# Performance work log

Measured on AMD Instinct MI355X. Metric: run time of the kernel, lower is better.

## Reference

```python
import jax, jax.numpy as jnp
import numpy as np

K = 5              # B-spline kernel size per dim
K3 = K ** 3        # 125 kernel weight slots
B = 32             # graphs per batch
NPG = [2048, 512, 128, 32, 8]   # nodes per graph at each level
DEG = 16           # average degree
RS = [0.1, 0.1, 0.125, 0.25, 0.5]  # CartesianAdj radii (1/10,1/10,2/16,2/8,2/4)


def _edges(rng, npg):
    # random edges, constrained within each graph
    E = B * npg * DEG
    g = np.repeat(np.arange(B) * npg, npg * DEG)
    src = g + rng.integers(0, npg, E)
    dst = g + rng.integers(0, npg, E)
    return jnp.asarray(np.stack([src, dst]), jnp.int32)


def _cluster(npg_prev, npg):
    # balanced voxel-cluster assignment within each graph (every cluster non-empty)
    n = np.arange(B * npg_prev)
    return jnp.asarray((n // npg_prev) * npg + (n % npg_prev) % npg, jnp.int32)


def setup_inputs() -> dict:
    key = jax.random.key(0)
    ks = iter(jax.random.split(key, 64))
    rng = np.random.default_rng(0)
    d = {}
    d['x0'] = jax.random.normal(next(ks), (B * NPG[0], 1), jnp.float32)
    d['pos0'] = jax.random.uniform(next(ks), (B * NPG[0], 3), jnp.float32) * 2.0
    chans = [1, 32, 64, 96, 128, 256]
    for i in range(5):
        ci, co = chans[i], chans[i + 1]
        s = 1.0 / np.sqrt(ci)
        d[f'W{i+1}'] = jax.random.normal(next(ks), (K3, ci, co), jnp.float32) * s
        d[f'root{i+1}'] = jax.random.normal(next(ks), (ci, co), jnp.float32) * s
        d[f'b{i+1}'] = jax.random.normal(next(ks), (co,), jnp.float32) * 0.01
    for i, c in enumerate([32, 64, 96, 128]):
        d[f'Wa{i+1}'] = jax.random.normal(next(ks), (c, 2), jnp.float32) / np.sqrt(c)
        d[f'ba{i+1}'] = jnp.zeros((2,), jnp.float32)
    d['Wfc'] = jax.random.normal(next(ks), (8 * 256, 10), jnp.float32) * 0.02
    d['bfc'] = jnp.zeros((10,), jnp.float32)
    for i in range(5):
        d[f'ei{i}'] = _edges(rng, NPG[i])
    for i in range(4):
        d[f'c{i+1}'] = _cluster(NPG[i], NPG[i + 1])
    return d


def _cartesian(pos, ei, r):
    # CartesianAdj: relative edge offsets scaled to [0,1]
    delta = pos[ei[1]] - pos[ei[0]]
    return jnp.clip(delta / (2.0 * r) + 0.5, 0.0, 1.0)


def _spline_conv(x, ei, pseudo, W, root, b):
    # SplineConv, degree-1 open B-splines, dim=3, kernel_size=5, mean aggregation
    src, dst = ei[0], ei[1]
    N, Cin = x.shape
    u = pseudo * (K - 1)                       # [E,3]
    k0f = jnp.clip(jnp.floor(u), 0.0, K - 2)
    frac = u - k0f
    k0 = k0f.astype(jnp.int32)
    xs = x[src]                                # [E,Cin]
    A = jnp.zeros((N, K3, Cin), x.dtype)       # basis-weighted aggregation buffer
    for bits in range(8):                      # 2^3 corners of the spline support
        off = np.array([(bits >> t) & 1 for t in range(3)])
        w = jnp.prod(jnp.where(off[None, :] == 1, frac, 1.0 - frac), axis=1)  # [E]
        kd = k0 + off[None, :]
        kidx = kd[:, 0] + K * kd[:, 1] + K * K * kd[:, 2]
        A = A.at[dst, kidx].add(w[:, None] * xs)
    out = jnp.einsum('nki,kio->no', A, W)
    deg = jnp.zeros((N,), x.dtype).at[dst].add(1.0)
    return out / jnp.maximum(deg, 1.0)[:, None] + x @ root + b


def _max_pool(x, weight, pos, cluster, nc):
    # attention-weighted sparse voxel max pool: keep node with max weight per voxel
    n = x.shape[0]
    m = jax.ops.segment_max(weight, cluster, nc)
    cand = jnp.where(weight >= m[cluster], jnp.arange(n), n)
    sel = jnp.minimum(jax.ops.segment_min(cand, cluster, nc), n - 1)
    cnt = jax.ops.segment_sum(jnp.ones((n,), pos.dtype), cluster, nc)
    ppos = jax.ops.segment_sum(pos, cluster, nc) / jnp.maximum(cnt, 1.0)[:, None]
    return x[sel], ppos


def _forward(x0, pos0, Ws, roots, bs, Was, bas, Wfc, bfc, eis, cs):
    x, pos = x0, pos0
    for i in range(4):
        ps = _cartesian(pos, eis[i], RS[i])
        x = jax.nn.elu(_spline_conv(x, eis[i], ps, Ws[i], roots[i], bs[i]))
        att = x @ Was[i] + bas[i]
        x, pos = _max_pool(x, att[:, 0], pos, cs[i], B * NPG[i + 1])
    ps = _cartesian(pos, eis[4], RS[4])
    x = jax.nn.elu(_spline_conv(x, eis[4], ps, Ws[4], roots[4], bs[4]))
    # dense_voxel_max_pool(data, 1, -0.5, 1.5): 2x2x2 voxels per graph
    vox = jnp.clip(jnp.floor(pos + 0.5), 0, 1).astype(jnp.int32)
    batch = jnp.arange(B * NPG[4], dtype=jnp.int32) // NPG[4]
    cl = batch * 8 + vox[:, 0] * 4 + vox[:, 1] * 2 + vox[:, 2]
    mx = jax.ops.segment_max(x, cl, B * 8)
    cnt = jax.ops.segment_sum(jnp.ones((x.shape[0],), x.dtype), cl, B * 8)
    mx = jnp.where(cnt[:, None] > 0, mx, 0.0)  # empty voxels -> 0
    logits = mx.reshape(B, 8 * 256) @ Wfc + bfc  # eval mode: dropout is identity
    return jax.nn.log_softmax(logits, axis=1)


def reference(x0, pos0, W1, root1, b1, W2, root2, b2, W3, root3, b3, W4, root4, b4, W5, root5, b5, Wa1, ba1, Wa2, ba2, Wa3, ba3, Wa4, ba4, Wfc, bfc, ei0, ei1, ei2, ei3, ei4, c1, c2, c3, c4):
    return _forward(x0, pos0, [W1, W2, W3, W4, W5], [root1, root2, root3, root4, root5],
                    [b1, b2, b3, b4, b5], [Wa1, Wa2, Wa3, Wa4], [ba1, ba2, ba3, ba4],
                    Wfc, bfc, [ei0, ei1, ei2, ei3, ei4], [c1, c2, c3, c4])
```

## Files before the change

kernel.cpp:

```cpp
#include <hip/hip_runtime.h>
#include <hip/hip_bf16.h>
#include <cstdint>
#include <cstddef>

#define KS 5
#define K3 125

typedef __attribute__((ext_vector_type(8))) short bf16x8;
typedef __attribute__((ext_vector_type(4))) float f32x4;

struct PreArgs {
    const int* src[5]; const int* dst[5];
    int* cnt[5]; int* slots[5];
    int npg[5];
    const float* W[5]; unsigned short* Wt[5];
    int Kd[5], KdP[5], Co[5];
    int fillFirst[6]; int wtFirst[6]; int ktiles[5];
};

__device__ __forceinline__ unsigned f2ord(float f){
    unsigned u = __float_as_uint(f);
    return (u & 0x80000000u) ? ~u : (u | 0x80000000u);
}
__device__ __forceinline__ float ord2f(unsigned u){
    unsigned b = (u & 0x80000000u) ? (u & 0x7FFFFFFFu) : ~u;
    return __uint_as_float(b);
}
__device__ __forceinline__ unsigned short f2bf(float f){
    unsigned u = __float_as_uint(f);
    u = (u + 0x7FFFu + ((u >> 16) & 1u)) >> 16;
    return (unsigned short)u;
}
__device__ __forceinline__ unsigned pk_bf16(float a, float b){
    __hip_bfloat162 p = __float22bfloat162_rn(make_float2(a, b));
    return *(unsigned*)&p;
}

__global__ __launch_bounds__(1024) void k_pre3(PreArgs a){
    __shared__ float smf[64*65];
    int b = blockIdx.x;
    int tid = threadIdx.x;
    if(b < a.fillFirst[5]){
        int l = 0;
        while(b >= a.fillFirst[l+1]) l++;
        int g = b - a.fillFirst[l];
        int npg = a.npg[l];
        int E1 = npg*16;
        int nbase = g*npg;
        int* cnt = (int*)smf;
        for(int i=tid; i<npg; i+=1024) cnt[i] = 0;
        __syncthreads();
        const int* srcp = a.src[l] + (size_t)g*E1;
        const int* dstp = a.dst[l] + (size_t)g*E1;
        int* slots = a.slots[l];
        for(int e=tid; e<E1; e+=1024){
            int d = dstp[e];
            int s = srcp[e];
            int p = __hip_atomic_fetch_add(&cnt[d - nbase], 1,
                        __ATOMIC_RELAXED, __HIP_MEMORY_SCOPE_WORKGROUP);
            if(p < 64) slots[(size_t)d*64 + p] = s;
        }
        __syncthreads();
        int* cg = a.cnt[l];
        for(int i=tid; i<npg; i+=1024) cg[nbase + i] = cnt[i];
        return;
    }
    int r = b - a.fillFirst[5];
    int l = 0;
    while(r >= a.wtFirst[l+1]) l++;
    int idx = r - a.wtFirst[l];
    int kb = (idx % a.ktiles[l])*64;
    int cb = (idx / a.ktiles[l])*64;
    int Kd = a.Kd[l], KdP = a.KdP[l], Co = a.Co[l];
    const float* W = a.W[l];
    unsigned short* Wt = a.Wt[l];
    float (*t)[65] = (float(*)[65])smf;
    int cc = tid & 63, rg = tid >> 6;
    #pragma unroll
    for(int i=0;i<4;i++){
        int kl = rg + i*16;
        int kk = kb + kl, co = cb + cc;
        t[kl][cc] = (kk < Kd && co < Co) ? W[(size_t)kk*Co + co] : 0.f;
    }
    __syncthreads();
    int kl = tid & 63;
    #pragma unroll
    for(int i=0;i<4;i++){
        int col = rg + i*16;
        int co = cb + col;
        int kk = kb + kl;
        if(co < Co && kk < KdP) Wt[(size_t)co*KdP + kk] = f2bf(t[kl][col]);
    }
}

__device__ __forceinline__ void spline_meta(float dx, float dy, float dz, float inv2r,
        float* wgt, int* ki){
    float fr[3]; int k0[3];
    float dd[3] = {dx, dy, dz};
    #pragma unroll
    for(int dim=0; dim<3; dim++){
        float p = dd[dim]*inv2r + 0.5f;
        p = fminf(fmaxf(p, 0.f), 1.f);
        float u = p*4.0f;
        float kf = fminf(floorf(u), 3.f);
        fr[dim] = u - kf; k0[dim] = (int)kf;
    }
    #pragma unroll
    for(int bits=0; bits<8; bits++){
        wgt[bits] = ((bits&1)? fr[0] : 1.f-fr[0])
                  * ((bits&2)? fr[1] : 1.f-fr[1])
                  * ((bits&4)? fr[2] : 1.f-fr[2]);
        ki[bits]  = (k0[0]+(bits&1)) + KS*(k0[1]+((bits>>1)&1)) + KS*KS*(k0[2]+((bits>>2)&1));
    }
}

__global__ __launch_bounds__(256) void k_build2(const int* __restrict__ slots,
        const int* __restrict__ cnt, const float* __restrict__ pos,
        const float* __restrict__ x,
        float inv2r, int n0, int Cin, int KdP, unsigned short* __restrict__ A){
    const int CH = 32;
    __shared__ float row[K3*32];
    __shared__ float xbuf[CH*32];
    __shared__ float ew[CH][8];
    __shared__ unsigned short bkt[16][CH];
    __shared__ int bcnt[16];
    __shared__ int esrc[CH];
    int tid = threadIdx.x;
    int node = n0 + blockIdx.x;
    int ci0 = blockIdx.y*32;
    for(int i=tid; i<K3*32; i+=256) row[i] = 0.f;
    int ecnt = min(cnt[node], 64);
    const int* sl = slots + (size_t)node*64;
    float pdx = pos[node*3+0], pdy = pos[node*3+1], pdz = pos[node*3+2];

    for(int c0=0; c0<ecnt; c0+=CH){
        int cc2 = min(CH, ecnt-c0);
        __syncthreads();
        if(tid < 16) bcnt[tid] = 0;
        float w[8]; int ki[8];
        if(tid < cc2){
            int s = sl[c0+tid];
            esrc[tid] = s;
            spline_meta(pdx-pos[s*3+0], pdy-pos[s*3+1], pdz-pos[s*3+2], inv2r, w, ki);
            #pragma unroll
            for(int b=0;b<8;b++) ew[tid][b] = w[b];
        }
        __syncthreads();
        if(tid < cc2){
            #pragma unroll
            for(int b=0;b<8;b++){
                int g = ki[b] & 15;
                int p = atomicAdd(&bcnt[g], 1);
                bkt[g][p] = (unsigned short)((ki[b]<<8) | (tid<<3) | b);
            }
        }
        for(int i=tid; i<cc2*32; i+=256){
            int e = i >> 5, ci = i & 31;
            xbuf[i] = x[(size_t)esrc[e]*Cin + ci0 + ci];
        }
        __syncthreads();
        int g  = tid >> 4;
        int cl = (tid & 15)*2;
        int ng = bcnt[g];
        for(int i=0; i<ng; i++){
            unsigned v = bkt[g][i];
            int kq = v >> 8;
            int e  = (v >> 3) & 31;
            float wv = ew[e][v & 7];
            float2 xv = *(float2*)&xbuf[e*32 + cl];
            float2* rp = (float2*)&row[kq*32 + cl];
            float2 rv = *rp;
            rv.x += wv*xv.x;
            rv.y += wv*xv.y;
            *rp = rv;
        }
    }
    __syncthreads();
    size_t gbase = (size_t)blockIdx.x*KdP + ci0;
    for(int i=tid*4; i<K3*32; i+=1024){
        int k = i >> 5, c = i & 31;
        uint2 pk;
        pk.x = pk_bf16(row[i],   row[i+1]);
        pk.y = pk_bf16(row[i+2], row[i+3]);
        *(uint2*)&A[gbase + (size_t)k*Cin + c] = pk;
    }
}

__global__ __launch_bounds__(256) void k_build1(const int* __restrict__ slots,
        const int* __restrict__ cnt, const float* __restrict__ pos,
        const float* __restrict__ x,
        float inv2r, int n0, int KdP, unsigned short* __restrict__ A){
    const int NB = 32, KD = K3;
    __shared__ float rows[NB*KD];
    int tid = threadIdx.x;
    for(int i=tid; i<NB*KD; i+=256) rows[i] = 0.f;
    __syncthreads();
    int nb = tid >> 3;
    int grp = tid & 7;
    int node = n0 + blockIdx.x*NB + nb;
    float* row = rows + nb*KD;
    float pdx = pos[node*3+0], pdy = pos[node*3+1], pdz = pos[node*3+2];
    int ecnt = min(cnt[node], 64);
    const int* sl = slots + (size_t)node*64;
    for(int ii=grp; ii<ecnt; ii+=8){
        int s = sl[ii];
        float w[8]; int ki[8];
        spline_meta(pdx-pos[s*3+0], pdy-pos[s*3+1], pdz-pos[s*3+2], inv2r, w, ki);
        float xs = x[s];
        #pragma unroll
        for(int b=0; b<8; b++)
            __hip_atomic_fetch_add(&row[ki[b]], w[b]*xs, __ATOMIC_RELAXED, __HIP_MEMORY_SCOPE_WORKGROUP);
    }
    __syncthreads();
    size_t gbase = (size_t)blockIdx.x*NB*KdP;
    int tot = NB*KdP;
    for(int i=tid*2; i<tot; i+=512){
        int nbw = i / KdP;
        int kk  = i - nbw*KdP;
        float v0 = (kk   < KD) ? rows[nbw*KD + kk]   : 0.f;
        float v1 = (kk+1 < KD) ? rows[nbw*KD + kk+1] : 0.f;
        *(unsigned*)&A[gbase + i] = pk_bf16(v0, v1);
    }
}

template<int BN>
__global__ __launch_bounds__(256) void k_mfma(const unsigned short* __restrict__ A,
        const unsigned short* __restrict__ Wt, float* __restrict__ acc,
        int n0, int Co, int KdP, int Kper){
    const int NBF = BN/16;
    __shared__ unsigned short Al[128*32];
    __shared__ unsigned short Bl[BN*32];
    int tid = threadIdx.x;
    int m0 = blockIdx.x*128, nb0 = blockIdx.y*BN;
    int kstart = blockIdx.z*Kper;
    int kend = min(KdP, kstart + Kper);
    if(kstart >= kend) return;
    int w = tid >> 6, l = tid & 63, lm = l & 15, lk = l >> 4;
    f32x4 c[2][NBF];
    #pragma unroll
    for(int i=0;i<2;i++)
        #pragma unroll
        for(int j=0;j<NBF;j++) c[i][j] = (f32x4){0,0,0,0};
    int ar = tid >> 1, ah = (tid & 1)*16;

    for(int k0=kstart; k0<kend; k0+=32){
        const unsigned short* ga = A + (size_t)(m0+ar)*KdP + k0 + ah;
        *(uint4*)&Al[ar*32 + ah]     = *(const uint4*)ga;
        *(uint4*)&Al[ar*32 + ah + 8] = *(const uint4*)(ga + 8);
        if(tid < BN*4){
            int bn = tid >> 2, bk = (tid & 3)*8;
            *(uint4*)&Bl[bn*32 + bk] = *(const uint4*)(Wt + (size_t)(nb0+bn)*KdP + k0 + bk);
        }
        __syncthreads();
        bf16x8 af[2], bfr[NBF];
        #pragma unroll
        for(int i=0;i<2;i++) af[i] = *(bf16x8*)&Al[(w*32 + i*16 + lm)*32 + lk*8];
        #pragma unroll
        for(int j=0;j<NBF;j++) bfr[j] = *(bf16x8*)&Bl[(j*16 + lm)*32 + lk*8];
        #pragma unroll
        for(int i=0;i<2;i++)
            #pragma unroll
            for(int j=0;j<NBF;j++)
                c[i][j] = __builtin_amdgcn_mfma_f32_16x16x32_bf16(af[i], bfr[j], c[i][j], 0,0,0);
        __syncthreads();
    }
    #pragma unroll
    for(int i=0;i<2;i++){
        int mb = n0 + m0 + w*32 + i*16 + lk*4;
        #pragma unroll
        for(int j=0;j<NBF;j++){
            int col = nb0 + j*16 + lm;
            if(gridDim.z == 1){
                #pragma unroll
                for(int r=0;r<4;r++) acc[(size_t)(mb+r)*Co + col] = c[i][j][r];
            } else {
                #pragma unroll
                for(int r=0;r<4;r++) atomicAdd(&acc[(size_t)(mb+r)*Co + col], c[i][j][r]);
            }
        }
    }
}

__global__ void k_finish2(const float* __restrict__ acc, const int* __restrict__ deg,
        const float* __restrict__ xin, const float* __restrict__ root,
        const float* __restrict__ bias, const float* __restrict__ Wa,
        const float* __restrict__ ba, float* __restrict__ y,
        const int* __restrict__ cl, const float* __restrict__ pin,
        unsigned long long* __restrict__ m_p, float* __restrict__ cntf,
        float* __restrict__ ppos, int N, int Cin, int Co, int NPB){
    extern __shared__ float sm[];
    float* xs  = sm;
    float* red = sm + NPB*Cin;
    int tid = threadIdx.x;
    int nl = tid / Co, co = tid - nl*Co;
    int n = blockIdx.x*NPB + nl;
    bool act = (n < N);
    if(act) for(int c=co; c<Cin; c+=Co) xs[nl*Cin + c] = xin[(size_t)n*Cin + c];
    __syncthreads();
    float yv = 0.f;
    if(act){
        float v = acc[(size_t)n*Co + co] / (float)max(deg[n], 1);
        float rt = 0.f;
        for(int c=0; c<Cin; c++) rt += xs[nl*Cin + c]*root[(size_t)c*Co + co];
        v += rt + bias[co];
        yv = v > 0.f ? v : expm1f(v);
        y[(size_t)n*Co + co] = yv;
    }
    if(m_p){
        float av = act ? yv * Wa[co*2] : 0.f;
        if(Co <= 64){
            #pragma unroll
            for(int off=32; off>0; off>>=1)
                if(off < Co) av += __shfl_xor(av, off, 64);
        } else {
            red[tid] = av;
            __syncthreads();
            int cur = Co;
            while(cur > 1){
                int half = (cur+1) >> 1;
                if(co < cur-half) red[nl*Co+co] += red[nl*Co+co+half];
                __syncthreads();
                cur = half;
            }
            av = red[nl*Co];
        }
        if(act && co==0){
            float attv = av + ba[0];
            int c = cl[n];
            unsigned long long pk = ((unsigned long long)f2ord(attv) << 32) | (unsigned)(~n);
            atomicMax(&m_p[c], pk);
            atomicAdd(&cntf[c], 1.f);
            atomicAdd(&ppos[c*3+0], pin[n*3+0]);
            atomicAdd(&ppos[c*3+1], pin[n*3+1]);
            atomicAdd(&ppos[c*3+2], pin[n*3+2]);
        }
    }
}

__global__ void k_pool3(const unsigned long long* __restrict__ m_p, const float* __restrict__ cntf,
        const float* __restrict__ ppos, const float* __restrict__ x,
        float* __restrict__ xo, float* __restrict__ poso, int nc, int Co, int nmax){
    int t = blockIdx.x*blockDim.x + threadIdx.x;
    if(t >= nc*Co) return;
    int c = t / Co;
    int co = t - c*Co;
    unsigned s = ~(unsigned)(m_p[c] & 0xFFFFFFFFull);
    s = min(s, (unsigned)(nmax-1));
    xo[(size_t)c*Co + co] = x[(size_t)s*Co + co];
    if(co < 3) poso[c*3+co] = ppos[c*3+co] / fmaxf(cntf[c], 1.f);
}

__global__ void k_vox(const float* __restrict__ x, const float* __restrict__ pos,
        unsigned* __restrict__ mx_u, float* __restrict__ cnt8){
    int nidx = blockIdx.x, ch = threadIdx.x;
    int v0 = min(max((int)floorf(pos[nidx*3+0]+0.5f),0),1);
    int v1 = min(max((int)floorf(pos[nidx*3+1]+0.5f),0),1);
    int v2 = min(max((int)floorf(pos[nidx*3+2]+0.5f),0),1);
    int b = nidx >> 3;
    int cl = b*8 + v0*4 + v1*2 + v2;
    atomicMax(&mx_u[cl*256+ch], f2ord(x[nidx*256+ch]));
    if(ch==0) atomicAdd(&cnt8[cl], 1.f);
}

__global__ __launch_bounds__(256) void k_fc(const unsigned* __restrict__ mx_u,
        const float* __restrict__ cnt8, const float* __restrict__ Wfc,
        const float* __restrict__ bfc, float* __restrict__ out){
    __shared__ float sred[10][256];
    int b = blockIdx.x, tid = threadIdx.x;
    float p[10];
    #pragma unroll
    for(int j=0;j<10;j++) p[j]=0.f;
    for(int idx=tid; idx<2048; idx+=256){
        int v = idx >> 8;
        float val = (cnt8[b*8+v] > 0.f) ? ord2f(mx_u[b*2048+idx]) : 0.f;
        const float* wr = &Wfc[idx*10];
        #pragma unroll
        for(int j=0;j<10;j++) p[j] += val*wr[j];
    }
    #pragma unroll
    for(int j=0;j<10;j++) sred[j][tid]=p[j];
    __syncthreads();
    for(int s=128;s>0;s>>=1){
        if(tid<s){
            #pragma unroll
            for(int j=0;j<10;j++) sred[j][tid]+=sred[j][tid+s];
        }
        __syncthreads();
    }
    if(tid==0){
        float lg[10], mx=-1e30f, se=0.f;
        for(int j=0;j<10;j++){ lg[j]=sred[j][0]+bfc[j]; mx=fmaxf(mx,lg[j]); }
        for(int j=0;j<10;j++) se += expf(lg[j]-mx);
        float lse = mx + logf(se);
        for(int j=0;j<10;j++) out[b*10+j] = lg[j]-lse;
    }
}

extern "C" void kernel_launch(void* const* d_in, const int* in_sizes, int n_in,
                              void* d_out, int out_size, void* d_ws, size_t ws_size,
                              hipStream_t stream){
    const float* x0   = (const float*)d_in[0];
    const float* pos0 = (const float*)d_in[1];
    const float *Wc[5], *rootc[5], *bc[5];
    for(int i=0;i<5;i++){
        Wc[i]    = (const float*)d_in[2+3*i];
        rootc[i] = (const float*)d_in[3+3*i];
        bc[i]    = (const float*)d_in[4+3*i];
    }
    const float *Wa[4], *ba[4];
    for(int i=0;i<4;i++){
        Wa[i] = (const float*)d_in[17+2*i];
        ba[i] = (const float*)d_in[18+2*i];
    }
    const float* Wfc = (const float*)d_in[25];
    const float* bfc = (const float*)d_in[26];
    const int* ei[5]; for(int i=0;i<5;i++) ei[i] = (const int*)d_in[27+i];
    const int* cl[4]; for(int i=0;i<4;i++) cl[i] = (const int*)d_in[32+i];

    const int NPG[5]   = {2048,512,128,32,8};
    const int chans[6] = {1,32,64,96,128,256};
    const float inv2r[5] = {5.f,5.f,4.f,2.f,1.f};
    const int B = 32;
    int Ns[5], Es[5], KdPs[5];
    int totN=0, totWt=0, accTotZ=0, poolTot=0;
    int nodeBase[5], wtBase[5], accOffZ[5], poolOff[4];
    for(int l=0;l<5;l++){
        Ns[l] = B*NPG[l]; Es[l] = Ns[l]*16;
        int Kd = K3*chans[l];
        KdPs[l] = (Kd + 31) & ~31;
        nodeBase[l] = totN; totN += Ns[l];
        wtBase[l] = totWt; totWt += chans[l+1]*KdPs[l];
        if(l >= 1){ accOffZ[l] = accTotZ; accTotZ += Ns[l]*chans[l+1]; }
    }
    for(int l=0;l<4;l++){ poolOff[l] = poolTot; poolTot += Ns[l+1]; }

    size_t off = 0;
    auto alloc = [&](size_t bytes)->void*{
        void* p = (char*)d_ws + off;
        off = (off + bytes + 255) & ~(size_t)255;
        return p;
    };
    float*    x_a    = (float*)   alloc((size_t)65536*32*4);
    float*    x_b    = (float*)   alloc((size_t)16384*32*4);
    float*    pos_a  = (float*)   alloc((size_t)16384*3*4);
    float*    pos_b  = (float*)   alloc((size_t)4096*3*4);
    float*    acc0   = (float*)   alloc((size_t)65536*32*4);
    int*      slots_a= (int*)     alloc((size_t)totN*64*4);
    int*      cnt_a  = (int*)     alloc((size_t)totN*4);
    unsigned short* Wt_a = (unsigned short*)alloc((size_t)totWt*2);
    size_t zstart = off;
    float*    accz_a = (float*)   alloc((size_t)accTotZ*4);
    unsigned long long* m_p_a = (unsigned long long*)alloc((size_t)poolTot*8);
    float*    cntf_a = (float*)   alloc((size_t)poolTot*4);
    float*    ppos_a = (float*)   alloc((size_t)poolTot*12);
    unsigned* mx_u   = (unsigned*)alloc((size_t)256*256*4);
    float*    cnt8   = (float*)   alloc((size_t)256*4);
    size_t zlen = off - zstart;
    unsigned short* A = (unsigned short*)((char*)d_ws + off);
    size_t Abudget = (ws_size > off) ? (ws_size - off) : 0;

    PreArgs pa;
    int wb = 0;
    for(int l=0;l<5;l++){
        pa.src[l] = ei[l];
        pa.dst[l] = ei[l] + Es[l];
        pa.cnt[l] = cnt_a + nodeBase[l];
        pa.slots[l] = slots_a + (size_t)nodeBase[l]*64;
        pa.npg[l] = NPG[l];
        pa.W[l] = Wc[l]; pa.Wt[l] = Wt_a + wtBase[l];
        pa.Kd[l] = K3*chans[l]; pa.KdP[l] = KdPs[l]; pa.Co[l] = chans[l+1];
        pa.fillFirst[l] = l*B;
        pa.ktiles[l] = (KdPs[l] + 63)/64;
        pa.wtFirst[l] = wb; wb += pa.ktiles[l] * ((chans[l+1] + 63)/64);
    }
    pa.fillFirst[5] = 5*B;
    pa.wtFirst[5] = wb;
    int preBlocks = 5*B + wb;

    hipMemsetAsync((char*)d_ws + zstart, 0, zlen, stream);
    k_pre3<<<preBlocks, 1024, 0, stream>>>(pa);

    const float* xin = x0;
    const float* pin = pos0;

    for(int L=0; L<5; L++){
        int N  = Ns[L];
        int Cin = chans[L], Co = chans[L+1];
        int KdP = KdPs[L];
        const int* cntL   = cnt_a + nodeBase[L];
        const int* slotsL = slots_a + (size_t)nodeBase[L]*64;
        const unsigned short* WtL = pa.Wt[L];
        float* accL = (L == 0) ? acc0 : (accz_a + accOffZ[L]);

        size_t nodeb = (size_t)KdP*2;
        int Mc = (int)(Abudget / nodeb);
        Mc = (Mc / 128) * 128;
        if(Mc < 128) Mc = 128;
        if(Mc > N) Mc = N;

        for(int rn0=0; rn0<N; rn0+=Mc){
            int rn1 = (rn0+Mc < N) ? rn0+Mc : N;
            int Mr  = rn1 - rn0;
            if(Cin==1)
                k_build1<<<Mr/32, 256, 0, stream>>>(slotsL, cntL, pin, xin, inv2r[L], rn0, KdP, A);
            else
                k_build2<<<dim3(Mr, Cin/32), 256, 0, stream>>>(slotsL, cntL, pin, xin,
                                                               inv2r[L], rn0, Cin, KdP, A);

            int BN = (Co % 64 == 0) ? 64 : 32;
            int gx = Mr/128, gy = Co/BN;
            int S = 768/(gx*gy);
            if(S < 1) S = 1;
            if(L == 0) S = 1;
            int maxS = KdP/32;
            if(S > maxS) S = maxS;
            int Kper = ((KdP + S - 1)/S + 31) & ~31;
            S = (KdP + Kper - 1)/Kper;
            dim3 g(gx, gy, S);
            if(BN == 64) k_mfma<64><<<g, 256, 0, stream>>>(A, WtL, accL, rn0, Co, KdP, Kper);
            else         k_mfma<32><<<g, 256, 0, stream>>>(A, WtL, accL, rn0, Co, KdP, Kper);
        }

        float* y = x_a;
        int NPB = 256/Co; if(NPB < 1) NPB = 1;
        int thr = NPB*Co;
        size_t smb = (size_t)(NPB*Cin + NPB*Co)*4;
        bool haspool = (L < 4);
        k_finish2<<<(N+NPB-1)/NPB, thr, smb, stream>>>(accL, cntL, xin, rootc[L], bc[L],
            haspool?Wa[L]:nullptr, haspool?ba[L]:nullptr, y,
            haspool?cl[L]:nullptr, pin,
            haspool?(m_p_a+poolOff[L]):nullptr,
            haspool?(cntf_a+poolOff[L]):nullptr,
            haspool?(ppos_a+(size_t)poolOff[L]*3):nullptr,
            N, Cin, Co, NPB);

        if(haspool){
            int nc = Ns[L+1];
            float* pout = (L%2==0) ? pos_a : pos_b;
            k_pool3<<<(nc*Co+255)/256, 256, 0, stream>>>(m_p_a+poolOff[L], cntf_a+poolOff[L],
                ppos_a+(size_t)poolOff[L]*3, y, x_b, pout, nc, Co, N);
            xin = x_b; pin = pout;
        }
    }

    k_vox<<<256, 256, 0, stream>>>(x_a, pin, mx_u, cnt8);
    k_fc<<<32, 256, 0, stream>>>(mx_u, cnt8, Wfc, bfc, (float*)d_out);
}
```

Measured before the change: 451.2 us.

## Bucket edge slots in shared memory per node sub-range and write coalesced

The preprocessing kernel's adjacency fill now splits each graph's nodes into sub-ranges: 8 for the 2048-node level and 2 for the 512-node level. Each block owns one sub-range and builds that range's neighbour slot lists in LDS. It then copies them to global memory with contiguous int4 stores, replacing per-edge scattered global writes. This raises the number of fill blocks and removes uncoalesced stores. In exchange, every sub-range block rereads all of its graph's edges, and each block uses a larger LDS allocation, which may limit occupancy.

```diff
diff --git a/kernel.cpp b/kernel.cpp
--- a/kernel.cpp
+++ b/kernel.cpp
@@ -12,7 +12,7 @@
 struct PreArgs {
     const int* src[5]; const int* dst[5];
     int* cnt[5]; int* slots[5];
-    int npg[5];
+    int npg[5]; int subs[5];
     const float* W[5]; unsigned short* Wt[5];
     int Kd[5], KdP[5], Co[5];
     int fillFirst[6]; int wtFirst[6]; int ktiles[5];
@@ -36,33 +36,45 @@
     return *(unsigned*)&p;
 }
 
-__global__ __launch_bounds__(1024) void k_pre3(PreArgs a){
-    __shared__ float smf[64*65];
+__global__ __launch_bounds__(1024) void k_pre4(PreArgs a){
+    __shared__ int sbuf[256*64 + 256];
     int b = blockIdx.x;
     int tid = threadIdx.x;
     if(b < a.fillFirst[5]){
         int l = 0;
         while(b >= a.fillFirst[l+1]) l++;
-        int g = b - a.fillFirst[l];
+        int j = b - a.fillFirst[l];
+        int subs = a.subs[l];
+        int g = j / subs;
+        int r = j - g*subs;
         int npg = a.npg[l];
+        int NPR = npg / subs;
         int E1 = npg*16;
-        int nbase = g*npg;
-        int* cnt = (int*)smf;
-        for(int i=tid; i<npg; i+=1024) cnt[i] = 0;
+        int nbase = g*npg + r*NPR;
+        int* scnt  = sbuf;
+        int* sslot = sbuf + 256;
+        for(int i=tid; i<NPR; i+=1024) scnt[i] = 0;
         __syncthreads();
         const int* srcp = a.src[l] + (size_t)g*E1;
         const int* dstp = a.dst[l] + (size_t)g*E1;
-        int* slots = a.slots[l];
+        int gn0 = g*npg;
         for(int e=tid; e<E1; e+=1024){
-            int d = dstp[e];
-            int s = srcp[e];
-            int p = __hip_atomic_fetch_add(&cnt[d - nbase], 1,
-                        __ATOMIC_RELAXED, __HIP_MEMORY_SCOPE_WORKGROUP);
-            if(p < 64) slots[(size_t)d*64 + p] = s;
-        }
-        __syncthreads();
-        int* cg = a.cnt[l];
-        for(int i=tid; i<npg; i+=1024) cg[nbase + i] = cnt[i];
+            int d = dstp[e] - nbase;
+            if((unsigned)d < (unsigned)NPR){
+                int s = srcp[e];
+                int p = __hip_atomic_fetch_add(&scnt[d], 1,
+                            __ATOMIC_RELAXED, __HIP_MEMORY_SCOPE_WORKGROUP);
+                if(p < 64) sslot[d*64 + p] = s;
+            }
+        }
+        __syncthreads();
+        int* gs = a.slots[l] + (size_t)nbase*64;
+        int tot = NPR*64;
+        for(int i=tid*4; i<tot; i+=4096)
+            *(int4*)&gs[i] = *(int4*)&sslot[i];
+        int* cg = a.cnt[l] + nbase;
+        for(int i=tid; i<NPR; i+=1024) cg[i] = scnt[i];
+        (void)gn0;
         return;
     }
     int r = b - a.fillFirst[5];
@@ -74,7 +86,7 @@
     int Kd = a.Kd[l], KdP = a.KdP[l], Co = a.Co[l];
     const float* W = a.W[l];
     unsigned short* Wt = a.Wt[l];
-    float (*t)[65] = (float(*)[65])smf;
+    float (*t)[65] = (float(*)[65])sbuf;
     int cc = tid & 63, rg = tid >> 6;
     #pragma unroll
     for(int i=0;i<4;i++){
@@ -421,6 +433,7 @@
     const int chans[6] = {1,32,64,96,128,256};
     const float inv2r[5] = {5.f,5.f,4.f,2.f,1.f};
     const int B = 32;
+    const int SUBS[5] = {8,2,1,1,1};
     int Ns[5], Es[5], KdPs[5];
     int totN=0, totWt=0, accTotZ=0, poolTot=0;
     int nodeBase[5], wtBase[5], accOffZ[5], poolOff[4];
@@ -460,25 +473,26 @@
     size_t Abudget = (ws_size > off) ? (ws_size - off) : 0;
 
     PreArgs pa;
-    int wb = 0;
+    int fb = 0, wb = 0;
     for(int l=0;l<5;l++){
         pa.src[l] = ei[l];
         pa.dst[l] = ei[l] + Es[l];
         pa.cnt[l] = cnt_a + nodeBase[l];
         pa.slots[l] = slots_a + (size_t)nodeBase[l]*64;
         pa.npg[l] = NPG[l];
+        pa.subs[l] = SUBS[l];
         pa.W[l] = Wc[l]; pa.Wt[l] = Wt_a + wtBase[l];
         pa.Kd[l] = K3*chans[l]; pa.KdP[l] = KdPs[l]; pa.Co[l] = chans[l+1];
-        pa.fillFirst[l] = l*B;
+        pa.fillFirst[l] = fb; fb += B*SUBS[l];
         pa.ktiles[l] = (KdPs[l] + 63)/64;
         pa.wtFirst[l] = wb; wb += pa.ktiles[l] * ((chans[l+1] + 63)/64);
     }
-    pa.fillFirst[5] = 5*B;
+    pa.fillFirst[5] = fb;
     pa.wtFirst[5] = wb;
-    int preBlocks = 5*B + wb;
+    int preBlocks = fb + wb;
 
     hipMemsetAsync((char*)d_ws + zstart, 0, zlen, stream);
-    k_pre3<<<preBlocks, 1024, 0, stream>>>(pa);
+    k_pre4<<<preBlocks, 1024, 0, stream>>>(pa);
 
     const float* xin = x0;
     const float* pin = pos0;
```

Result: faster. 438.9 us (-2.7%).
